# Optimization experiments

Hardware: AMD Instinct MI355X
Metric: run time of the kernel (lower is better)

Reference implementation:

```python
import jax, jax.numpy as jnp
import numpy as np

B, N, IN_F, OUT_F = 2, 4096, 256, 256
ALPHA = 0.2          # LeakyReLU negative slope
MASK_NEG = -9e15     # zero_vec fill for non-edges
SINK_NEG = -1e9      # small_tensor sink column


def setup_inputs() -> dict:
    key = jax.random.key(0)
    kx, kadj, kw, kbw, kai, kbi, kaj, kbj = jax.random.split(key, 8)
    x = jax.random.normal(kx, (B, N, IN_F), dtype=jnp.float32)
    adjs = (jax.random.uniform(kadj, (B, N, N)) < 0.01).astype(jnp.float32)
    # xavier_uniform with gain=1.414 for Linear weights (shape [out, in])
    def xavier(k, shape, gain=1.414):
        fan_out, fan_in = shape
        bound = gain * np.sqrt(6.0 / (fan_in + fan_out))
        return jax.random.uniform(k, shape, minval=-bound, maxval=bound, dtype=jnp.float32)
    W = xavier(kw, (OUT_F, IN_F))
    bW = jax.random.uniform(kbw, (OUT_F,), minval=-1/np.sqrt(IN_F), maxval=1/np.sqrt(IN_F), dtype=jnp.float32)
    wai = xavier(kai, (1, OUT_F))
    bai = jax.random.uniform(kbi, (1,), minval=-1/np.sqrt(OUT_F), maxval=1/np.sqrt(OUT_F), dtype=jnp.float32)
    waj = xavier(kaj, (1, OUT_F))
    baj = jax.random.uniform(kbj, (1,), minval=-1/np.sqrt(OUT_F), maxval=1/np.sqrt(OUT_F), dtype=jnp.float32)
    return {"x": x, "adjs": adjs, "W": W, "bW": bW,
            "wai": wai, "bai": bai, "waj": waj, "baj": baj}


def reference(x, adjs, W, bW, wai, bai, waj, baj):
    b, n, _ = adjs.shape
    z = jnp.einsum('bni,oi->bno', x, W) + bW                 # [B,N,OUT]
    ai = jnp.einsum('bno,ko->bnk', z, wai) + bai             # [B,N,1]
    aj = jnp.einsum('bno,ko->bnk', z, waj) + baj             # [B,N,1]
    # [ai,1] @ [1,aj]^T == ai_i + aj_j (broadcast add)
    e = ai + jnp.swapaxes(aj, 1, 2)                          # [B,N,N]
    e = jnp.where(e >= 0, e, ALPHA * e)                      # LeakyReLU
    att = jnp.where(adjs > 0, e, MASK_NEG)                   # adjacency mask
    # sink column trick: append -1e9 logit, softmax over N+1, drop sink
    sink = jnp.full((b, n, 1), SINK_NEG, dtype=att.dtype)
    att = jax.nn.softmax(jnp.concatenate([att, sink], axis=-1), axis=-1)[:, :, :n]
    # dropout p=0 in eval -> identity
    return jnp.einsum('bnm,bmo->bno', att, z)                # [B,N,OUT]
```

## Files before the change

kernel.cpp:

```cpp
#include <hip/hip_runtime.h>
#include <hip/hip_bf16.h>


#define NN   4096
#define OUTF 256
#define INF  256
#define CAP_E 128

typedef __attribute__((ext_vector_type(8))) short short8v;
typedef __attribute__((ext_vector_type(4))) float f32x4;

static __device__ __forceinline__ unsigned short f2bf(float f) {
    union { float f; unsigned u; } v; v.f = f;
    unsigned r = v.u + 0x7fffu + ((v.u >> 16) & 1u);
    return (unsigned short)(r >> 16);
}
static __device__ __forceinline__ float bf2f(unsigned short u) {
    union { unsigned u; float f; } v; v.u = ((unsigned)u) << 16; return v.f;
}

#define BM 64
#define BN 64
#define BK 64

__global__ __launch_bounds__(256) void gat_zgemm(
        const float* __restrict__ x, const float* __restrict__ W,
        const float* __restrict__ bW, const float* __restrict__ wai,
        const float* __restrict__ waj, unsigned short* __restrict__ zb,
        float* __restrict__ pai, float* __restrict__ paj,
        const float* __restrict__ adj, unsigned short* __restrict__ mask16) {
    __shared__ alignas(16) unsigned short As[BM * BK];
    __shared__ alignas(16) unsigned short Bs[BN * BK];
    const int tid  = threadIdx.x;
    const int lane = tid & 63;
    const int wid  = tid >> 6;
    const int rowBase = blockIdx.x * BM;
    const int colBase = blockIdx.y * BN;
    const int wm = (wid >> 1) * 32;
    const int wn = (wid & 1) * 32;
    const int sr = tid >> 4;
    const int sc = tid & 15;

    f32x4 acc[2][2] = {};

    for (int kk = 0; kk < INF; kk += BK) {
        #pragma unroll
        for (int pass = 0; pass < BM / 16; ++pass) {
            int r = pass * 16 + sr;
            const float4 v = *(const float4*)(&x[(size_t)(rowBase + r) * INF + kk + sc * 4]);
            int off = r * 128 + ((sc * 8) ^ ((r & 7) << 4));
            *(ushort4*)((char*)As + off) =
                make_ushort4(f2bf(v.x), f2bf(v.y), f2bf(v.z), f2bf(v.w));
        }
        #pragma unroll
        for (int pass = 0; pass < BN / 16; ++pass) {
            int r = pass * 16 + sr;
            const float4 v = *(const float4*)(&W[(size_t)(colBase + r) * INF + kk + sc * 4]);
            int off = r * 128 + ((sc * 8) ^ ((r & 7) << 4));
            *(ushort4*)((char*)Bs + off) =
                make_ushort4(f2bf(v.x), f2bf(v.y), f2bf(v.z), f2bf(v.w));
        }
        __syncthreads();
        #pragma unroll
        for (int ks = 0; ks < 2; ++ks) {
            short8v aF[2], bF[2];
            #pragma unroll
            for (int m = 0; m < 2; ++m) {
                int row = wm + m * 16 + (lane & 15);
                int cb  = (ks * 64 + ((lane >> 4) * 16)) ^ ((row & 7) << 4);
                aF[m] = *(const short8v*)((const char*)As + row * 128 + cb);
            }
            #pragma unroll
            for (int n = 0; n < 2; ++n) {
                int row = wn + n * 16 + (lane & 15);
                int cb  = (ks * 64 + ((lane >> 4) * 16)) ^ ((row & 7) << 4);
                bF[n] = *(const short8v*)((const char*)Bs + row * 128 + cb);
            }
            #pragma unroll
            for (int m = 0; m < 2; ++m)
                #pragma unroll
                for (int n = 0; n < 2; ++n)
                    acc[m][n] = __builtin_amdgcn_mfma_f32_16x16x32_bf16(
                        aF[m], bF[n], acc[m][n], 0, 0, 0);
        }
        __syncthreads();
    }
    {
        const int r4 = (lane >> 4) * 4;
        const int cW = lane & 15;
        const int col0 = colBase + wn + cW;
        const int col1 = col0 + 16;
        const float b0 = bW[col0],  b1 = bW[col1];
        const float i0 = wai[col0], i1 = wai[col1];
        const float j0 = waj[col0], j1 = waj[col1];
        const int slot = blockIdx.y * 2 + (wid & 1);
        #pragma unroll
        for (int m = 0; m < 2; ++m) {
            #pragma unroll
            for (int r = 0; r < 4; ++r) {
                int row = rowBase + wm + m * 16 + r4 + r;
                float z0 = acc[m][0][r] + b0;
                float z1 = acc[m][1][r] + b1;
                zb[(size_t)row * OUTF + col0] = f2bf(z0);
                zb[(size_t)row * OUTF + col1] = f2bf(z1);
                float pi = z0 * i0 + z1 * i1;
                float pj = z0 * j0 + z1 * j1;
                #pragma unroll
                for (int s = 1; s < 16; s <<= 1) {
                    pi += __shfl_xor(pi, s);
                    pj += __shfl_xor(pj, s);
                }
                if (cW == 0) {
                    pai[row * 8 + slot] = pi;
                    paj[row * 8 + slot] = pj;
                }
            }
        }
    }

    {
        const int bid = blockIdx.y * gridDim.x + blockIdx.x;
        const size_t fbase = (size_t)bid * 65536;
        #pragma unroll 2
        for (int it = 0; it < 16; ++it) {
            size_t F = fbase + (size_t)it * 4096 + wid * 1024 + lane * 16;
            unsigned bits = 0;
            #pragma unroll
            for (int q = 0; q < 4; ++q) {
                const float4 v = *(const float4*)(adj + F + q * 4);
                bits |= (v.x > 0.f ? 1u : 0u) << (q * 4);
                bits |= (v.y > 0.f ? 2u : 0u) << (q * 4);
                bits |= (v.z > 0.f ? 4u : 0u) << (q * 4);
                bits |= (v.w > 0.f ? 8u : 0u) << (q * 4);
            }
            mask16[F >> 4] = (unsigned short)bits;
        }
    }
}

__global__ __launch_bounds__(256) void gat_attend(
        const unsigned long long* __restrict__ mask64,
        const float* __restrict__ pai, const float* __restrict__ paj,
        const float* __restrict__ bai, const float* __restrict__ baj,
        const unsigned short* __restrict__ zb, float* __restrict__ out) {
    __shared__ unsigned short s_idx[4][CAP_E];
    __shared__ float          s_w[4][CAP_E];
    const int tid  = threadIdx.x;
    const int lane = tid & 63;
    const int wv   = tid >> 6;
    const int row  = blockIdx.x * 4 + wv;
    const int b    = row >> 12;
    unsigned short* si = s_idx[wv];
    float* swv = s_w[wv];

    unsigned long long mm = mask64[(size_t)row * 64 + lane];
    const int c = __popcll(mm);
    int incl = c;
    #pragma unroll
    for (int s = 1; s < 64; s <<= 1) {
        int t = __shfl_up(incl, s);
        if (lane >= s) incl += t;
    }
    const int cnt0 = __shfl(incl, 63);
    const int cnt = cnt0 > CAP_E ? CAP_E : cnt0;
    int pos = incl - c;
    while (mm) {
        int bit = __builtin_ctzll(mm);
        if (pos < CAP_E) si[pos] = (unsigned short)(lane * 64 + bit);
        ++pos;
        mm &= mm - 1;
    }

    const float4* pa = (const float4*)(pai + row * 8);
    const float4 u = pa[0], v2 = pa[1];
    const float AI = (u.x + u.y + u.z + u.w) + (v2.x + v2.y + v2.z + v2.w)
                   + bai[0] + baj[0];

    const bool h0 = lane < cnt, h1 = lane + 64 < cnt;
    float a0 = -3e38f, a1 = -3e38f;
    const float* pjb = paj + ((size_t)(b << 12)) * 8;
    if (h0) {
        const float4* q = (const float4*)(pjb + si[lane] * 8);
        float4 x0 = q[0], x1 = q[1];
        a0 = (x0.x + x0.y + x0.z + x0.w) + (x1.x + x1.y + x1.z + x1.w);
    }
    if (h1) {
        const float4* q = (const float4*)(pjb + si[lane + 64] * 8);
        float4 x0 = q[0], x1 = q[1];
        a1 = (x0.x + x0.y + x0.z + x0.w) + (x1.x + x1.y + x1.z + x1.w);
    }
    float lm = fmaxf(a0, a1);
    #pragma unroll
    for (int s = 1; s < 64; s <<= 1) lm = fmaxf(lm, __shfl_xor(lm, s));
    const float tm = AI + lm;
    const float m = tm >= 0.f ? tm : 0.2f * tm;
    float w0 = 0.f, w1 = 0.f;
    if (h0) { float e = AI + a0; e = e >= 0.f ? e : 0.2f * e; w0 = __expf(e - m); }
    if (h1) { float e = AI + a1; e = e >= 0.f ? e : 0.2f * e; w1 = __expf(e - m); }
    float ls = w0 + w1;
    #pragma unroll
    for (int s = 1; s < 64; s <<= 1) ls += __shfl_xor(ls, s);
    const float inv = cnt ? 1.f / ls : 0.f;
    if (h0) swv[lane] = w0;
    if (h1) swv[lane + 64] = w1;

    const unsigned short* zcol = zb + ((size_t)(b << 12)) * OUTF + lane * 4;
    float4 acc = make_float4(0.f, 0.f, 0.f, 0.f);
    int p = 0;
    for (; p + 4 <= cnt; p += 4) {
        int   g0 = si[p],  g1 = si[p + 1], g2 = si[p + 2], g3 = si[p + 3];
        float W0 = swv[p], W1 = swv[p + 1], W2 = swv[p + 2], W3 = swv[p + 3];
        ushort4 q0 = *(const ushort4*)(zcol + (size_t)g0 * OUTF);
        ushort4 q1 = *(const ushort4*)(zcol + (size_t)g1 * OUTF);
        ushort4 q2 = *(const ushort4*)(zcol + (size_t)g2 * OUTF);
        ushort4 q3 = *(const ushort4*)(zcol + (size_t)g3 * OUTF);
        acc.x = fmaf(W0, bf2f(q0.x), fmaf(W1, bf2f(q1.x), fmaf(W2, bf2f(q2.x), fmaf(W3, bf2f(q3.x), acc.x))));
        acc.y = fmaf(W0, bf2f(q0.y), fmaf(W1, bf2f(q1.y), fmaf(W2, bf2f(q2.y), fmaf(W3, bf2f(q3.y), acc.y))));
        acc.z = fmaf(W0, bf2f(q0.z), fmaf(W1, bf2f(q1.z), fmaf(W2, bf2f(q2.z), fmaf(W3, bf2f(q3.z), acc.z))));
        acc.w = fmaf(W0, bf2f(q0.w), fmaf(W1, bf2f(q1.w), fmaf(W2, bf2f(q2.w), fmaf(W3, bf2f(q3.w), acc.w))));
    }
    for (; p < cnt; ++p) {
        int g = si[p]; float Wp = swv[p];
        ushort4 q = *(const ushort4*)(zcol + (size_t)g * OUTF);
        acc.x = fmaf(Wp, bf2f(q.x), acc.x);
        acc.y = fmaf(Wp, bf2f(q.y), acc.y);
        acc.z = fmaf(Wp, bf2f(q.z), acc.z);
        acc.w = fmaf(Wp, bf2f(q.w), acc.w);
    }
    *(float4*)(out + (size_t)row * OUTF + lane * 4) =
        make_float4(acc.x * inv, acc.y * inv, acc.z * inv, acc.w * inv);
}

extern "C" void kernel_launch(void* const* d_in, const int* in_sizes, int n_in,
                              void* d_out, int out_size, void* d_ws, size_t ws_size,
                              hipStream_t stream) {
    const float* x   = (const float*)d_in[0];
    const float* adj = (const float*)d_in[1];
    const float* W   = (const float*)d_in[2];
    const float* bW  = (const float*)d_in[3];
    const float* wai = (const float*)d_in[4];
    const float* bai = (const float*)d_in[5];
    const float* waj = (const float*)d_in[6];
    const float* baj = (const float*)d_in[7];
    float* out = (float*)d_out;

    char* ws = (char*)d_ws;
    unsigned short* zb   = (unsigned short*)ws;
    float* pai = (float*)(ws + (4u << 20));
    float* paj = pai + 8192 * 8;
    unsigned short* mask = (unsigned short*)(ws + (5u << 20));

    gat_zgemm<<<dim3(8192 / BM, OUTF / BN), 256, 0, stream>>>(
        x, W, bW, wai, waj, zb, pai, paj, adj, mask);
    gat_attend<<<2048, 256, 0, stream>>>(
        (const unsigned long long*)mask, pai, paj, bai, baj, zb, out);
}
```

Measured before the change: 54.58 us.

## Split adjacency bitmask packing into separate blocks using wave ballots

```diff
diff --git a/kernel.cpp b/kernel.cpp
--- a/kernel.cpp
+++ b/kernel.cpp
@@ -22,20 +22,42 @@
 #define BM 64
 #define BN 64
 #define BK 64
-
-__global__ __launch_bounds__(256) void gat_zgemm(
+#define GEMM_BLOCKS 512
+#define MASK_BLOCKS 2048
+
+__global__ __launch_bounds__(256) void gat_pre(
         const float* __restrict__ x, const float* __restrict__ W,
         const float* __restrict__ bW, const float* __restrict__ wai,
         const float* __restrict__ waj, unsigned short* __restrict__ zb,
         float* __restrict__ pai, float* __restrict__ paj,
-        const float* __restrict__ adj, unsigned short* __restrict__ mask16) {
+        const float* __restrict__ adj, unsigned long long* __restrict__ mask64) {
     __shared__ alignas(16) unsigned short As[BM * BK];
     __shared__ alignas(16) unsigned short Bs[BN * BK];
     const int tid  = threadIdx.x;
     const int lane = tid & 63;
     const int wid  = tid >> 6;
-    const int rowBase = blockIdx.x * BM;
-    const int colBase = blockIdx.y * BN;
+
+    if (blockIdx.x >= GEMM_BLOCKS) {
+        const int widx = (blockIdx.x - GEMM_BLOCKS) * 4 + wid;
+        const float4* a4 = (const float4*)adj;
+        const size_t cbase = (size_t)widx * 16;
+        #pragma unroll 4
+        for (int c = 0; c < 16; ++c) {
+            const float4 v = a4[(cbase + c) * 64 + lane];
+            unsigned long long b0 = __ballot(v.x > 0.f);
+            unsigned long long b1 = __ballot(v.y > 0.f);
+            unsigned long long b2 = __ballot(v.z > 0.f);
+            unsigned long long b3 = __ballot(v.w > 0.f);
+            if (lane == 0) {
+                unsigned long long* dst = mask64 + (cbase + c) * 4;
+                dst[0] = b0; dst[1] = b1; dst[2] = b2; dst[3] = b3;
+            }
+        }
+        return;
+    }
+
+    const int rowBase = (blockIdx.x & 127) * BM;
+    const int colBase = (blockIdx.x >> 7) * BN;
     const int wm = (wid >> 1) * 32;
     const int wn = (wid & 1) * 32;
     const int sr = tid >> 4;
@@ -85,55 +107,34 @@
         }
         __syncthreads();
     }
-    {
-        const int r4 = (lane >> 4) * 4;
-        const int cW = lane & 15;
-        const int col0 = colBase + wn + cW;
-        const int col1 = col0 + 16;
-        const float b0 = bW[col0],  b1 = bW[col1];
-        const float i0 = wai[col0], i1 = wai[col1];
-        const float j0 = waj[col0], j1 = waj[col1];
-        const int slot = blockIdx.y * 2 + (wid & 1);
-        #pragma unroll
-        for (int m = 0; m < 2; ++m) {
-            #pragma unroll
-            for (int r = 0; r < 4; ++r) {
-                int row = rowBase + wm + m * 16 + r4 + r;
-                float z0 = acc[m][0][r] + b0;
-                float z1 = acc[m][1][r] + b1;
-                zb[(size_t)row * OUTF + col0] = f2bf(z0);
-                zb[(size_t)row * OUTF + col1] = f2bf(z1);
-                float pi = z0 * i0 + z1 * i1;
-                float pj = z0 * j0 + z1 * j1;
-                #pragma unroll
-                for (int s = 1; s < 16; s <<= 1) {
-                    pi += __shfl_xor(pi, s);
-                    pj += __shfl_xor(pj, s);
-                }
-                if (cW == 0) {
-                    pai[row * 8 + slot] = pi;
-                    paj[row * 8 + slot] = pj;
-                }
-            }
-        }
-    }
-
-    {
-        const int bid = blockIdx.y * gridDim.x + blockIdx.x;
-        const size_t fbase = (size_t)bid * 65536;
-        #pragma unroll 2
-        for (int it = 0; it < 16; ++it) {
-            size_t F = fbase + (size_t)it * 4096 + wid * 1024 + lane * 16;
-            unsigned bits = 0;
-            #pragma unroll
-            for (int q = 0; q < 4; ++q) {
-                const float4 v = *(const float4*)(adj + F + q * 4);
-                bits |= (v.x > 0.f ? 1u : 0u) << (q * 4);
-                bits |= (v.y > 0.f ? 2u : 0u) << (q * 4);
-                bits |= (v.z > 0.f ? 4u : 0u) << (q * 4);
-                bits |= (v.w > 0.f ? 8u : 0u) << (q * 4);
-            }
-            mask16[F >> 4] = (unsigned short)bits;
+    const int r4 = (lane >> 4) * 4;
+    const int cW = lane & 15;
+    const int col0 = colBase + wn + cW;
+    const int col1 = col0 + 16;
+    const float b0 = bW[col0],  b1 = bW[col1];
+    const float i0 = wai[col0], i1 = wai[col1];
+    const float j0 = waj[col0], j1 = waj[col1];
+    const int slot = (blockIdx.x >> 7) * 2 + (wid & 1);
+    #pragma unroll
+    for (int m = 0; m < 2; ++m) {
+        #pragma unroll
+        for (int r = 0; r < 4; ++r) {
+            int row = rowBase + wm + m * 16 + r4 + r;
+            float z0 = acc[m][0][r] + b0;
+            float z1 = acc[m][1][r] + b1;
+            zb[(size_t)row * OUTF + col0] = f2bf(z0);
+            zb[(size_t)row * OUTF + col1] = f2bf(z1);
+            float pi = z0 * i0 + z1 * i1;
+            float pj = z0 * j0 + z1 * j1;
+            #pragma unroll
+            for (int s = 1; s < 16; s <<= 1) {
+                pi += __shfl_xor(pi, s);
+                pj += __shfl_xor(pj, s);
+            }
+            if (cW == 0) {
+                pai[row * 8 + slot] = pi;
+                paj[row * 8 + slot] = pj;
+            }
         }
     }
 }
@@ -164,9 +165,10 @@
     const int cnt0 = __shfl(incl, 63);
     const int cnt = cnt0 > CAP_E ? CAP_E : cnt0;
     int pos = incl - c;
+    const int jbase = (lane >> 2) * 256 + (lane & 3);
     while (mm) {
         int bit = __builtin_ctzll(mm);
-        if (pos < CAP_E) si[pos] = (unsigned short)(lane * 64 + bit);
+        if (pos < CAP_E) si[pos] = (unsigned short)(jbase + bit * 4);
         ++pos;
         mm &= mm - 1;
     }
@@ -248,10 +250,10 @@
     unsigned short* zb   = (unsigned short*)ws;
     float* pai = (float*)(ws + (4u << 20));
     float* paj = pai + 8192 * 8;
-    unsigned short* mask = (unsigned short*)(ws + (5u << 20));
-
-    gat_zgemm<<<dim3(8192 / BM, OUTF / BN), 256, 0, stream>>>(
+    unsigned long long* mask = (unsigned long long*)(ws + (5u << 20));
+
+    gat_pre<<<GEMM_BLOCKS + MASK_BLOCKS, 256, 0, stream>>>(
         x, W, bW, wai, waj, zb, pai, paj, adj, mask);
     gat_attend<<<2048, 256, 0, stream>>>(
-        (const unsigned long long*)mask, pai, paj, bai, baj, zb, out);
-}
+        mask, pai, paj, bai, baj, zb, out);
+}
```

New measurement: 45.43 us. 1.2x faster.
